# Performance work log

Hardware: AMD Instinct MI355X
Metric: run time of the kernel (lower is better)

## Reference

```python
import jax, jax.numpy as jnp
import numpy as np

ATTEN = 2  # window half-size -> 2*ATTEN+1 = 5 neighbors
B, S, IN, H, MID, OUT = 1024, 100, 100, 128, 32, 2
MAX_LEN = 100
SQRT_H = float(np.sqrt(float(H)))


def _xavier(k, i, o):
    return jax.random.normal(k, (i, o), jnp.float32) * np.sqrt(2.0 / (i + o))


def _positional_encoding():
    pos = np.arange(MAX_LEN, dtype=np.float32)[:, None]
    div = np.exp(np.arange(0, H, 2, dtype=np.float32) * (-np.log(10000.0) / H))
    pe = np.zeros((MAX_LEN, H), np.float32)
    pe[:, 0::2] = np.sin(pos * div)
    pe[:, 1::2] = np.cos(pos * div)
    return jnp.asarray(pe[None])  # (1, MAX_LEN, H)


def setup_inputs() -> dict:
    key = jax.random.key(0)
    ks = jax.random.split(key, 7)
    return {
        "x": jax.random.normal(ks[0], (B, S, IN), jnp.float32),
        "W1": _xavier(ks[1], IN, H),
        "b1": jnp.zeros((1, 1, H), jnp.float32),
        "Wq": _xavier(ks[2], H, H),
        "Wk": _xavier(ks[3], H, H),
        "Wv": _xavier(ks[4], H, H),
        "bv": jnp.zeros((1, 1, H), jnp.float32),
        "W2": _xavier(ks[5], H, MID),
        "b2": jnp.zeros((1, 1, MID), jnp.float32),
        "W3": _xavier(ks[6], MID, OUT),
        "b3": jnp.zeros((1, 1, OUT), jnp.float32),
        "pe": _positional_encoding(),
    }


def reference(x, W1, b1, Wq, Wk, Wv, bv, W2, b2, W3, b3, pe):
    seq_len = x.shape[1]
    h = jax.nn.relu(x @ W1 + b1) + pe[:, :seq_len, :]  # (B,S,H)
    # zero-pad seq dim by ATTEN on each side; torch pad+roll+stack+slice is
    # equivalent to gathering window offsets +2,+1,0,-1,-2 (in that order)
    padded = jnp.pad(h, ((0, 0), (ATTEN, ATTEN), (0, 0)))
    x_nei = jnp.stack(
        [padded[:, ATTEN - k: ATTEN - k + seq_len, :] for k in range(-ATTEN, ATTEN + 1)],
        axis=2,
    )  # (B,S,5,H); index m corresponds to neighbor x[i + ATTEN - m]
    q = h @ Wq                      # (B,S,H)
    keys = x_nei @ Wk               # (B,S,5,H)
    vals = x_nei @ Wv + bv          # (B,S,5,H)
    scores = jnp.einsum("bsh,bswh->bsw", q, keys) / SQRT_H
    w = jax.nn.softmax(scores, axis=-1)  # (B,S,5)
    context = jnp.einsum("bsw,bswh->bsh", w, vals)
    output = jax.nn.relu(context @ W2 + b2) @ W3 + b3  # (B,S,OUT)
    return output, w[:, :, None, :]  # weights shaped (B,S,1,5) like torch
```

## Files before the change

### kernel.cpp

```cpp
#include <hip/hip_runtime.h>
#include <hip/hip_bf16.h>

#define B_ 1024
#define S_ 100
#define IN_ 100
#define H_ 128
#define MID_ 32
#define OUT_ 2
#define P_ (B_ * S_)
#define RSQRT_H 0.08838834764831845f
#define LSTR 136
#define TILE 25
#define KR 32
#define HR 36
#define HTS 40
#define SSTR 36
#define WSTR 40

typedef __attribute__((ext_vector_type(8))) short short8;
typedef __attribute__((ext_vector_type(4))) float float4v;

__device__ __forceinline__ float bf2f(ushort u) {
    union { unsigned u; float f; } c; c.u = ((unsigned)u) << 16; return c.f;
}
__device__ __forceinline__ ushort f2bf(float x) {
    union { float f; unsigned u; } c; c.f = x;
    unsigned r = c.u + 0x7FFFu + ((c.u >> 16) & 1u);
    return (ushort)(r >> 16);
}

__global__ __launch_bounds__(256) void prep_kernel(const float* __restrict__ W1,
                                                   const float* __restrict__ Wv,
                                                   const float* __restrict__ W2,
                                                   const float* __restrict__ Wq,
                                                   const float* __restrict__ Wk,
                                                   ushort* __restrict__ W1T,
                                                   ushort* __restrict__ WvT,
                                                   ushort* __restrict__ W2T,
                                                   ushort* __restrict__ WqkT) {
    int tid = threadIdx.x;
    if (blockIdx.x < 144) {
        int g = blockIdx.x * 256 + tid;
        if (g < 16384) {
            int n = g >> 7, k = g & 127;
            W1T[g] = (k < IN_) ? f2bf(W1[k * H_ + n]) : (ushort)0;
        } else if (g < 32768) {
            int e = g - 16384; int n = e >> 7, k = e & 127;
            WvT[e] = f2bf(Wv[k * H_ + n]);
        } else {
            int e = g - 32768; int n = e >> 7, k = e & 127;
            W2T[e] = f2bf(W2[k * MID_ + n]);
        }
    } else {
        __shared__ float sq[32][132];
        __shared__ float sk[32][132];
        int bb = blockIdx.x - 144;
        int n0 = (bb >> 2) * 32, k0 = (bb & 3) * 32;
        for (int i = tid; i < 32 * 128; i += 256) {
            int r = i >> 7, c = i & 127;
            sq[r][c] = Wq[(k0 + r) * H_ + c];
            sk[r][c] = Wk[(n0 + r) * H_ + c];
        }
        __syncthreads();
        for (int i = tid; i < 1024; i += 256) {
            int kk = i & 31, nn = i >> 5;
            float a = 0.f;
            for (int j = 0; j < 128; ++j) a += sq[kk][j] * sk[nn][j];
            WqkT[(n0 + nn) * 128 + (k0 + kk)] = f2bf(a * RSQRT_H);
        }
    }
}

template <int EPI, bool HT>
__device__ __forceinline__ void mm2(const ushort* __restrict__ A, int abase,
                                    const ushort* __restrict__ WT,
                                    ushort* __restrict__ C,
                                    ushort* __restrict__ hTp,
                                    int wave, int lane,
                                    const float* __restrict__ bias,
                                    const float* __restrict__ pe, int srow0) {
    int l15 = lane & 15, quad = lane >> 4;
    short8 bfrag[2][4];
#pragma unroll
    for (int nt = 0; nt < 2; ++nt) {
        int n = (wave * 2 + nt) * 16 + l15;
#pragma unroll
        for (int ks = 0; ks < 4; ++ks)
            bfrag[nt][ks] = *(const short8*)(WT + n * 128 + ks * 32 + quad * 8);
    }
    float biasv[2] = {0.f, 0.f};
    if (EPI != 0) {
#pragma unroll
        for (int nt = 0; nt < 2; ++nt) biasv[nt] = bias[(wave * 2 + nt) * 16 + l15];
    }
#pragma unroll
    for (int mt = 0; mt < 2; ++mt) {
        short8 afrag[4];
#pragma unroll
        for (int ks = 0; ks < 4; ++ks)
            afrag[ks] = *(const short8*)(A + (abase + mt * 16 + l15) * LSTR + ks * 32 + quad * 8);
#pragma unroll
        for (int nt = 0; nt < 2; ++nt) {
            float4v acc = {0.f, 0.f, 0.f, 0.f};
#pragma unroll
            for (int ks = 0; ks < 4; ++ks)
                acc = __builtin_amdgcn_mfma_f32_16x16x32_bf16(afrag[ks], bfrag[nt][ks], acc, 0, 0, 0);
            int n = (wave * 2 + nt) * 16 + l15;
#pragma unroll
            for (int i = 0; i < 4; ++i) {
                int row = mt * 16 + quad * 4 + i;
                float v = acc[i];
                if (EPI == 1) {
                    int srow = srow0 + row;
                    v = (srow >= 0 && srow < S_)
                            ? (fmaxf(v + biasv[nt], 0.f) + pe[srow * H_ + n]) : 0.f;
                } else if (EPI == 2) v = v + biasv[nt];
                ushort bf = f2bf(v);
                C[row * LSTR + n] = bf;
                if (HT) hTp[n * HTS + row] = bf;
            }
        }
    }
}

__global__ __launch_bounds__(256, 4) void fused_kernel(
    const float* __restrict__ x, const ushort* __restrict__ W1T,
    const ushort* __restrict__ WqkT, const ushort* __restrict__ WvT,
    const ushort* __restrict__ W2T,
    const float* __restrict__ b1, const float* __restrict__ bv,
    const float* __restrict__ b2, const float* __restrict__ W3,
    const float* __restrict__ b3, const float* __restrict__ pe,
    float* __restrict__ out, float* __restrict__ wout) {
    __shared__ __attribute__((aligned(16))) ushort klds[KR * LSTR];
    __shared__ __attribute__((aligned(16))) ushort hlds[HR * LSTR];
    __shared__ __attribute__((aligned(16))) ushort hT[H_ * HTS];
    __shared__ __attribute__((aligned(16))) float  slds[KR * SSTR];
    __shared__ __attribute__((aligned(16))) ushort wband[KR * WSTR];
    __shared__ float warr[TILE * 5];

    int tid = threadIdx.x, wave = tid >> 6, lane = tid & 63;
    int l15 = lane & 15, quad = lane >> 4;
    int b = blockIdx.x >> 2, t = blockIdx.x & 3;
    int r0 = t * TILE;
    int srow0 = r0 - 2;

    for (int i = tid; i < 29 * 18; i += 256) {
        int r = i / 18, c = 100 + 2 * (i - r * 18);
        *(uint*)(klds + r * LSTR + c) = 0u;
    }
    for (int i = tid; i < 3 * 68; i += 256) {
        int r = 29 + i / 68, c = 2 * (i % 68);
        *(uint*)(klds + r * LSTR + c) = 0u;
    }
    for (int i = tid; i < 4 * 68; i += 256) {
        int r = 32 + i / 68, c = 2 * (i % 68);
        *(uint*)(hlds + r * LSTR + c) = 0u;
    }
    {
        int g0 = srow0 < 0 ? 0 : srow0;
        int g1 = (r0 + 27 < S_) ? (r0 + 27) : S_;
        int lr0 = g0 - srow0;
        const float* xb = x + ((size_t)b * S_ + g0) * IN_;
        int pairs = (g1 - g0) * 50;
        for (int p = tid; p < pairs; p += 256) {
            int row = p / 50;
            int c2 = (p - row * 50) * 2;
            const float* src = xb + row * IN_ + c2;
            uint pk = ((uint)f2bf(src[1]) << 16) | (uint)f2bf(src[0]);
            *(uint*)(klds + (lr0 + row) * LSTR + c2) = pk;
        }
    }
    __syncthreads();
    mm2<1, true>(klds, 0, W1T, hlds, hT, wave, lane, b1, pe, srow0);
    __syncthreads();
    mm2<0, false>(hlds, 2, WqkT, klds, nullptr, wave, lane, nullptr, nullptr, 0);
    __syncthreads();
    if (wave < 3) {
        int qt = (wave == 2) ? 1 : 0;
        int ht = (wave == 0) ? 0 : 1;
        short8 afrag[4], bfrag[4];
#pragma unroll
        for (int ks = 0; ks < 4; ++ks) {
            afrag[ks] = *(const short8*)(klds + (qt * 16 + l15) * LSTR + ks * 32 + quad * 8);
            bfrag[ks] = *(const short8*)(hlds + (ht * 16 + l15) * LSTR + ks * 32 + quad * 8);
        }
        float4v acc = {0.f, 0.f, 0.f, 0.f};
#pragma unroll
        for (int ks = 0; ks < 4; ++ks)
            acc = __builtin_amdgcn_mfma_f32_16x16x32_bf16(afrag[ks], bfrag[ks], acc, 0, 0, 0);
#pragma unroll
        for (int i = 0; i < 4; ++i)
            slds[(qt * 16 + quad * 4 + i) * SSTR + ht * 16 + l15] = acc[i];
    } else {
        uint* wz = (uint*)wband;
        for (int i = lane; i < (KR * WSTR) / 2; i += 64) wz[i] = 0u;
    }
    __syncthreads();
    if (tid < TILE) {
        int i = tid;
        float sc5[5];
#pragma unroll
        for (int d = 0; d < 5; ++d) sc5[d] = slds[i * SSTR + i + d];
        float mx = sc5[0];
#pragma unroll
        for (int d = 1; d < 5; ++d) mx = fmaxf(mx, sc5[d]);
        float e5[5], ss = 0.f;
#pragma unroll
        for (int d = 0; d < 5; ++d) { e5[d] = __expf(sc5[d] - mx); ss += e5[d]; }
        float inv = 1.f / ss;
#pragma unroll
        for (int d = 0; d < 5; ++d) {
            float w = e5[d] * inv;
            wband[i * WSTR + i + d] = f2bf(w);
            warr[i * 5 + (4 - d)] = w;
        }
    }
    __syncthreads();
    {
        short8 afr[2];
        afr[0] = *(const short8*)(wband + l15 * WSTR + quad * 8);
        afr[1] = *(const short8*)(wband + (16 + l15) * WSTR + quad * 8);
#pragma unroll
        for (int ntt = 0; ntt < 2; ++ntt) {
            int n = (wave * 2 + ntt) * 16 + l15;
            short8 bfr = *(const short8*)(hT + n * HTS + quad * 8);
#pragma unroll
            for (int mt = 0; mt < 2; ++mt) {
                float4v acc = {0.f, 0.f, 0.f, 0.f};
                acc = __builtin_amdgcn_mfma_f32_16x16x32_bf16(afr[mt], bfr, acc, 0, 0, 0);
#pragma unroll
                for (int i = 0; i < 4; ++i)
                    klds[(mt * 16 + quad * 4 + i) * LSTR + n] = f2bf(acc[i]);
            }
        }
    }
    __syncthreads();
    mm2<2, false>(klds, 0, WvT, hlds, nullptr, wave, lane, bv, nullptr, 0);
    __syncthreads();
    if (tid < TILE * 5)
        wout[(size_t)b * (S_ * 5) + r0 * 5 + tid] = warr[tid];
    {
        int mt = wave & 1, nt = wave >> 1;
        short8 bfrag[4];
#pragma unroll
        for (int ks = 0; ks < 4; ++ks)
            bfrag[ks] = *(const short8*)(W2T + (nt * 16 + l15) * 128 + ks * 32 + quad * 8);
        float bias2 = b2[nt * 16 + l15];
        short8 afrag[4];
#pragma unroll
        for (int ks = 0; ks < 4; ++ks)
            afrag[ks] = *(const short8*)(hlds + (mt * 16 + l15) * LSTR + ks * 32 + quad * 8);
        float4v acc = {0.f, 0.f, 0.f, 0.f};
#pragma unroll
        for (int ks = 0; ks < 4; ++ks)
            acc = __builtin_amdgcn_mfma_f32_16x16x32_bf16(afrag[ks], bfrag[ks], acc, 0, 0, 0);
#pragma unroll
        for (int i = 0; i < 4; ++i) {
            int row = mt * 16 + quad * 4 + i;
            klds[row * LSTR + nt * 16 + l15] = f2bf(fmaxf(acc[i] + bias2, 0.f));
        }
    }
    __syncthreads();
    if (tid < TILE * 2) {
        int r = tid >> 1, c = tid & 1;
        float o = b3[c];
        const ushort* mr = klds + r * LSTR;
#pragma unroll
        for (int cs = 0; cs < 4; ++cs) {
            short8 v = *(const short8*)(mr + cs * 8);
#pragma unroll
            for (int j = 0; j < 8; ++j) o += bf2f((ushort)v[j]) * W3[(cs * 8 + j) * 2 + c];
        }
        out[((size_t)b * S_ + r0 + r) * OUT_ + c] = o;
    }
}

extern "C" void kernel_launch(void* const* d_in, const int* in_sizes, int n_in,
                              void* d_out, int out_size, void* d_ws, size_t ws_size,
                              hipStream_t stream) {
    const float* x  = (const float*)d_in[0];
    const float* W1 = (const float*)d_in[1];
    const float* b1 = (const float*)d_in[2];
    const float* Wq = (const float*)d_in[3];
    const float* Wk = (const float*)d_in[4];
    const float* Wv = (const float*)d_in[5];
    const float* bv = (const float*)d_in[6];
    const float* W2 = (const float*)d_in[7];
    const float* b2 = (const float*)d_in[8];
    const float* W3 = (const float*)d_in[9];
    const float* b3 = (const float*)d_in[10];
    const float* pe = (const float*)d_in[11];

    float* out  = (float*)d_out;
    float* wout = out + (size_t)P_ * OUT_;

    ushort* W1T  = (ushort*)d_ws;
    ushort* WqkT = W1T + 16384;
    ushort* WvT  = WqkT + 16384;
    ushort* W2T  = WvT + 16384;

    prep_kernel<<<160, 256, 0, stream>>>(W1, Wv, W2, Wq, Wk, W1T, WvT, W2T, WqkT);
    fused_kernel<<<B_ * 4, 256, 0, stream>>>(x, W1T, WqkT, WvT, W2T,
                                             b1, bv, b2, W3, b3, pe, out, wout);
}
```

Measured before the change: 168.2 us.

## Fold Wv into W2, fuse softmax and context per wave, vectorize loads

Precomputes Wv·W2 and bv·W2+b2 in the prep kernel, so the per-tile 128x128 value projection is dropped and the context feeds straight into the 32-wide MID layer. Scores, softmax and the banded context matmul now run inside two waves with no block barriers in between. The scores matrix is cut to the needed diagonal band and weights are written straight to global memory. Also vectorizes the x load with float4, packs the hT transposed stores, and shrinks LDS padding strides. Folding the matrices changes bf16 rounding slightly, and the stride changes may alter LDS bank conflicts.

```diff
diff --git a/kernel.cpp b/kernel.cpp
--- a/kernel.cpp
+++ b/kernel.cpp
@@ -9,13 +9,13 @@
 #define OUT_ 2
 #define P_ (B_ * S_)
 #define RSQRT_H 0.08838834764831845f
-#define LSTR 136
+#define LSTR 132
 #define TILE 25
 #define KR 32
-#define HR 36
-#define HTS 40
-#define SSTR 36
-#define WSTR 40
+#define HR 34
+#define HTS 36
+#define WSTR 36
+#define SSC 20
 
 typedef __attribute__((ext_vector_type(8))) short short8;
 typedef __attribute__((ext_vector_type(4))) float float4v;
@@ -30,31 +30,25 @@
 }
 
 __global__ __launch_bounds__(256) void prep_kernel(const float* __restrict__ W1,
+                                                   const float* __restrict__ Wq,
+                                                   const float* __restrict__ Wk,
                                                    const float* __restrict__ Wv,
                                                    const float* __restrict__ W2,
-                                                   const float* __restrict__ Wq,
-                                                   const float* __restrict__ Wk,
+                                                   const float* __restrict__ bv,
+                                                   const float* __restrict__ b2,
                                                    ushort* __restrict__ W1T,
-                                                   ushort* __restrict__ WvT,
-                                                   ushort* __restrict__ W2T,
-                                                   ushort* __restrict__ WqkT) {
+                                                   ushort* __restrict__ WqkT,
+                                                   ushort* __restrict__ Wvw2T,
+                                                   float* __restrict__ bv2) {
     int tid = threadIdx.x;
-    if (blockIdx.x < 144) {
+    if (blockIdx.x < 64) {
         int g = blockIdx.x * 256 + tid;
-        if (g < 16384) {
-            int n = g >> 7, k = g & 127;
-            W1T[g] = (k < IN_) ? f2bf(W1[k * H_ + n]) : (ushort)0;
-        } else if (g < 32768) {
-            int e = g - 16384; int n = e >> 7, k = e & 127;
-            WvT[e] = f2bf(Wv[k * H_ + n]);
-        } else {
-            int e = g - 32768; int n = e >> 7, k = e & 127;
-            W2T[e] = f2bf(W2[k * MID_ + n]);
-        }
-    } else {
+        int n = g >> 7, k = g & 127;
+        W1T[g] = (k < IN_) ? f2bf(W1[k * H_ + n]) : (ushort)0;
+    } else if (blockIdx.x < 80) {
         __shared__ float sq[32][132];
         __shared__ float sk[32][132];
-        int bb = blockIdx.x - 144;
+        int bb = blockIdx.x - 64;
         int n0 = (bb >> 2) * 32, k0 = (bb & 3) * 32;
         for (int i = tid; i < 32 * 128; i += 256) {
             int r = i >> 7, c = i & 127;
@@ -67,6 +61,18 @@
             float a = 0.f;
             for (int j = 0; j < 128; ++j) a += sq[kk][j] * sk[nn][j];
             WqkT[(n0 + nn) * 128 + (k0 + kk)] = f2bf(a * RSQRT_H);
+        }
+    } else if (blockIdx.x < 96) {
+        int e = (blockIdx.x - 80) * 256 + tid;
+        int n = e >> 7, k = e & 127;
+        float a = 0.f;
+        for (int j = 0; j < 128; ++j) a += Wv[k * H_ + j] * W2[j * MID_ + n];
+        Wvw2T[e] = f2bf(a);
+    } else {
+        if (tid < MID_) {
+            float a = b2[tid];
+            for (int j = 0; j < 128; ++j) a += bv[j] * W2[j * MID_ + tid];
+            bv2[tid] = a;
         }
     }
 }
@@ -89,7 +95,7 @@
             bfrag[nt][ks] = *(const short8*)(WT + n * 128 + ks * 32 + quad * 8);
     }
     float biasv[2] = {0.f, 0.f};
-    if (EPI != 0) {
+    if (EPI == 1) {
 #pragma unroll
         for (int nt = 0; nt < 2; ++nt) biasv[nt] = bias[(wave * 2 + nt) * 16 + l15];
     }
@@ -106,6 +112,7 @@
             for (int ks = 0; ks < 4; ++ks)
                 acc = __builtin_amdgcn_mfma_f32_16x16x32_bf16(afrag[ks], bfrag[nt][ks], acc, 0, 0, 0);
             int n = (wave * 2 + nt) * 16 + l15;
+            ushort bfv[4];
 #pragma unroll
             for (int i = 0; i < 4; ++i) {
                 int row = mt * 16 + quad * 4 + i;
@@ -114,10 +121,15 @@
                     int srow = srow0 + row;
                     v = (srow >= 0 && srow < S_)
                             ? (fmaxf(v + biasv[nt], 0.f) + pe[srow * H_ + n]) : 0.f;
-                } else if (EPI == 2) v = v + biasv[nt];
-                ushort bf = f2bf(v);
-                C[row * LSTR + n] = bf;
-                if (HT) hTp[n * HTS + row] = bf;
+                }
+                bfv[i] = f2bf(v);
+                C[row * LSTR + n] = bfv[i];
+            }
+            if (HT) {
+                uint2 pk;
+                pk.x = (uint)bfv[0] | ((uint)bfv[1] << 16);
+                pk.y = (uint)bfv[2] | ((uint)bfv[3] << 16);
+                *(uint2*)(hTp + n * HTS + mt * 16 + quad * 4) = pk;
             }
         }
     }
@@ -125,18 +137,16 @@
 
 __global__ __launch_bounds__(256, 4) void fused_kernel(
     const float* __restrict__ x, const ushort* __restrict__ W1T,
-    const ushort* __restrict__ WqkT, const ushort* __restrict__ WvT,
-    const ushort* __restrict__ W2T,
-    const float* __restrict__ b1, const float* __restrict__ bv,
-    const float* __restrict__ b2, const float* __restrict__ W3,
+    const ushort* __restrict__ WqkT, const ushort* __restrict__ Wvw2T,
+    const float* __restrict__ bv2,
+    const float* __restrict__ b1, const float* __restrict__ W3,
     const float* __restrict__ b3, const float* __restrict__ pe,
     float* __restrict__ out, float* __restrict__ wout) {
     __shared__ __attribute__((aligned(16))) ushort klds[KR * LSTR];
     __shared__ __attribute__((aligned(16))) ushort hlds[HR * LSTR];
     __shared__ __attribute__((aligned(16))) ushort hT[H_ * HTS];
-    __shared__ __attribute__((aligned(16))) float  slds[KR * SSTR];
     __shared__ __attribute__((aligned(16))) ushort wband[KR * WSTR];
-    __shared__ float warr[TILE * 5];
+    __shared__ __attribute__((aligned(16))) float  sscr[2][16][SSC];
 
     int tid = threadIdx.x, wave = tid >> 6, lane = tid & 63;
     int l15 = lane & 15, quad = lane >> 4;
@@ -144,30 +154,43 @@
     int r0 = t * TILE;
     int srow0 = r0 - 2;
 
-    for (int i = tid; i < 29 * 18; i += 256) {
-        int r = i / 18, c = 100 + 2 * (i - r * 18);
+    for (int i = tid; i < 29 * 14; i += 256) {
+        int r = i / 14, c = 100 + 2 * (i - r * 14);
         *(uint*)(klds + r * LSTR + c) = 0u;
     }
-    for (int i = tid; i < 3 * 68; i += 256) {
-        int r = 29 + i / 68, c = 2 * (i % 68);
+    for (int i = tid; i < 3 * 66; i += 256) {
+        int r = 29 + i / 66, c = 2 * (i % 66);
         *(uint*)(klds + r * LSTR + c) = 0u;
     }
-    for (int i = tid; i < 4 * 68; i += 256) {
-        int r = 32 + i / 68, c = 2 * (i % 68);
+    for (int i = tid; i < 2 * 66; i += 256) {
+        int r = 32 + i / 66, c = 2 * (i % 66);
         *(uint*)(hlds + r * LSTR + c) = 0u;
     }
+    for (int i = tid; i < (KR * WSTR) / 2; i += 256)
+        ((uint*)wband)[i] = 0u;
+
     {
         int g0 = srow0 < 0 ? 0 : srow0;
         int g1 = (r0 + 27 < S_) ? (r0 + 27) : S_;
         int lr0 = g0 - srow0;
         const float* xb = x + ((size_t)b * S_ + g0) * IN_;
-        int pairs = (g1 - g0) * 50;
-        for (int p = tid; p < pairs; p += 256) {
-            int row = p / 50;
-            int c2 = (p - row * 50) * 2;
-            const float* src = xb + row * IN_ + c2;
-            uint pk = ((uint)f2bf(src[1]) << 16) | (uint)f2bf(src[0]);
-            *(uint*)(klds + (lr0 + row) * LSTR + c2) = pk;
+        int quads = (g1 - g0) * 25;
+        float4 v[3];
+#pragma unroll
+        for (int it = 0; it < 3; ++it) {
+            int p = tid + it * 256;
+            if (p < quads) v[it] = *(const float4*)(xb + (p / 25) * IN_ + (p % 25) * 4);
+        }
+#pragma unroll
+        for (int it = 0; it < 3; ++it) {
+            int p = tid + it * 256;
+            if (p < quads) {
+                int row = p / 25, qr = p - row * 25;
+                uint2 pk;
+                pk.x = (uint)f2bf(v[it].x) | ((uint)f2bf(v[it].y) << 16);
+                pk.y = (uint)f2bf(v[it].z) | ((uint)f2bf(v[it].w) << 16);
+                *(uint2*)(klds + (lr0 + row) * LSTR + qr * 4) = pk;
+            }
         }
     }
     __syncthreads();
@@ -175,81 +198,73 @@
     __syncthreads();
     mm2<0, false>(hlds, 2, WqkT, klds, nullptr, wave, lane, nullptr, nullptr, 0);
     __syncthreads();
-    if (wave < 3) {
-        int qt = (wave == 2) ? 1 : 0;
-        int ht = (wave == 0) ? 0 : 1;
-        short8 afrag[4], bfrag[4];
-#pragma unroll
-        for (int ks = 0; ks < 4; ++ks) {
+    if (wave < 2) {
+        int qt = wave;
+        short8 afrag[4];
+#pragma unroll
+        for (int ks = 0; ks < 4; ++ks)
             afrag[ks] = *(const short8*)(klds + (qt * 16 + l15) * LSTR + ks * 32 + quad * 8);
-            bfrag[ks] = *(const short8*)(hlds + (ht * 16 + l15) * LSTR + ks * 32 + quad * 8);
-        }
-        float4v acc = {0.f, 0.f, 0.f, 0.f};
-#pragma unroll
-        for (int ks = 0; ks < 4; ++ks)
-            acc = __builtin_amdgcn_mfma_f32_16x16x32_bf16(afrag[ks], bfrag[ks], acc, 0, 0, 0);
-#pragma unroll
-        for (int i = 0; i < 4; ++i)
-            slds[(qt * 16 + quad * 4 + i) * SSTR + ht * 16 + l15] = acc[i];
-    } else {
-        uint* wz = (uint*)wband;
-        for (int i = lane; i < (KR * WSTR) / 2; i += 64) wz[i] = 0u;
-    }
-    __syncthreads();
-    if (tid < TILE) {
-        int i = tid;
-        float sc5[5];
-#pragma unroll
-        for (int d = 0; d < 5; ++d) sc5[d] = slds[i * SSTR + i + d];
-        float mx = sc5[0];
-#pragma unroll
-        for (int d = 1; d < 5; ++d) mx = fmaxf(mx, sc5[d]);
-        float e5[5], ss = 0.f;
-#pragma unroll
-        for (int d = 0; d < 5; ++d) { e5[d] = __expf(sc5[d] - mx); ss += e5[d]; }
-        float inv = 1.f / ss;
-#pragma unroll
-        for (int d = 0; d < 5; ++d) {
-            float w = e5[d] * inv;
-            wband[i * WSTR + i + d] = f2bf(w);
-            warr[i * 5 + (4 - d)] = w;
-        }
-    }
-    __syncthreads();
-    {
-        short8 afr[2];
-        afr[0] = *(const short8*)(wband + l15 * WSTR + quad * 8);
-        afr[1] = *(const short8*)(wband + (16 + l15) * WSTR + quad * 8);
-#pragma unroll
-        for (int ntt = 0; ntt < 2; ++ntt) {
-            int n = (wave * 2 + ntt) * 16 + l15;
-            short8 bfr = *(const short8*)(hT + n * HTS + quad * 8);
-#pragma unroll
-            for (int mt = 0; mt < 2; ++mt) {
-                float4v acc = {0.f, 0.f, 0.f, 0.f};
-                acc = __builtin_amdgcn_mfma_f32_16x16x32_bf16(afr[mt], bfr, acc, 0, 0, 0);
-#pragma unroll
-                for (int i = 0; i < 4; ++i)
-                    klds[(mt * 16 + quad * 4 + i) * LSTR + n] = f2bf(acc[i]);
-            }
-        }
-    }
-    __syncthreads();
-    mm2<2, false>(klds, 0, WvT, hlds, nullptr, wave, lane, bv, nullptr, 0);
-    __syncthreads();
-    if (tid < TILE * 5)
-        wout[(size_t)b * (S_ * 5) + r0 * 5 + tid] = warr[tid];
+#pragma unroll
+        for (int ht = 0; ht < 2; ++ht) {
+            if (ht < qt) continue;
+            short8 bfrag[4];
+#pragma unroll
+            for (int ks = 0; ks < 4; ++ks)
+                bfrag[ks] = *(const short8*)(hlds + (ht * 16 + l15) * LSTR + ks * 32 + quad * 8);
+            float4v acc = {0.f, 0.f, 0.f, 0.f};
+#pragma unroll
+            for (int ks = 0; ks < 4; ++ks)
+                acc = __builtin_amdgcn_mfma_f32_16x16x32_bf16(afrag[ks], bfrag[ks], acc, 0, 0, 0);
+            int c = (ht - qt) * 16 + l15;
+            if (c < SSC) {
+#pragma unroll
+                for (int i = 0; i < 4; ++i) sscr[qt][quad * 4 + i][c] = acc[i];
+            }
+        }
+        int nq = (qt == 0) ? 16 : 9;
+        if (lane < nq) {
+            int q = qt * 16 + lane;
+            float sc5[5];
+#pragma unroll
+            for (int d = 0; d < 5; ++d) sc5[d] = sscr[qt][lane][lane + d];
+            float mx = sc5[0];
+#pragma unroll
+            for (int d = 1; d < 5; ++d) mx = fmaxf(mx, sc5[d]);
+            float e5[5], ss = 0.f;
+#pragma unroll
+            for (int d = 0; d < 5; ++d) { e5[d] = __expf(sc5[d] - mx); ss += e5[d]; }
+            float inv = 1.f / ss;
+            float* wp = wout + ((size_t)b * S_ + r0 + q) * 5;
+#pragma unroll
+            for (int d = 0; d < 5; ++d) {
+                float w = e5[d] * inv;
+                wband[q * WSTR + q + d] = f2bf(w);
+                wp[4 - d] = w;
+            }
+        }
+        short8 wfrag = *(const short8*)(wband + (qt * 16 + l15) * WSTR + quad * 8);
+#pragma unroll
+        for (int nt2 = 0; nt2 < 8; ++nt2) {
+            short8 bfr = *(const short8*)(hT + (nt2 * 16 + l15) * HTS + quad * 8);
+            float4v acc = {0.f, 0.f, 0.f, 0.f};
+            acc = __builtin_amdgcn_mfma_f32_16x16x32_bf16(wfrag, bfr, acc, 0, 0, 0);
+#pragma unroll
+            for (int i = 0; i < 4; ++i)
+                klds[(qt * 16 + quad * 4 + i) * LSTR + nt2 * 16 + l15] = f2bf(acc[i]);
+        }
+    }
+    __syncthreads();
     {
         int mt = wave & 1, nt = wave >> 1;
         short8 bfrag[4];
 #pragma unroll
         for (int ks = 0; ks < 4; ++ks)
-            bfrag[ks] = *(const short8*)(W2T + (nt * 16 + l15) * 128 + ks * 32 + quad * 8);
-        float bias2 = b2[nt * 16 + l15];
+            bfrag[ks] = *(const short8*)(Wvw2T + (nt * 16 + l15) * 128 + ks * 32 + quad * 8);
+        float bias2 = bv2[nt * 16 + l15];
         short8 afrag[4];
 #pragma unroll
         for (int ks = 0; ks < 4; ++ks)
-            afrag[ks] = *(const short8*)(hlds + (mt * 16 + l15) * LSTR + ks * 32 + quad * 8);
+            afrag[ks] = *(const short8*)(klds + (mt * 16 + l15) * LSTR + ks * 32 + quad * 8);
         float4v acc = {0.f, 0.f, 0.f, 0.f};
 #pragma unroll
         for (int ks = 0; ks < 4; ++ks)
@@ -257,21 +272,21 @@
 #pragma unroll
         for (int i = 0; i < 4; ++i) {
             int row = mt * 16 + quad * 4 + i;
-            klds[row * LSTR + nt * 16 + l15] = f2bf(fmaxf(acc[i] + bias2, 0.f));
+            hlds[row * LSTR + nt * 16 + l15] = f2bf(fmaxf(acc[i] + bias2, 0.f));
         }
     }
     __syncthreads();
     if (tid < TILE * 2) {
-        int r = tid >> 1, c = tid & 1;
-        float o = b3[c];
-        const ushort* mr = klds + r * LSTR;
+        int r = tid >> 1, cc = tid & 1;
+        float o = b3[cc];
+        const ushort* mr = hlds + r * LSTR;
 #pragma unroll
         for (int cs = 0; cs < 4; ++cs) {
             short8 v = *(const short8*)(mr + cs * 8);
 #pragma unroll
-            for (int j = 0; j < 8; ++j) o += bf2f((ushort)v[j]) * W3[(cs * 8 + j) * 2 + c];
-        }
-        out[((size_t)b * S_ + r0 + r) * OUT_ + c] = o;
+            for (int j = 0; j < 8; ++j) o += bf2f((ushort)v[j]) * W3[(cs * 8 + j) * 2 + cc];
+        }
+        out[((size_t)b * S_ + r0 + r) * OUT_ + cc] = o;
     }
 }
 
@@ -294,12 +309,13 @@
     float* out  = (float*)d_out;
     float* wout = out + (size_t)P_ * OUT_;
 
-    ushort* W1T  = (ushort*)d_ws;
-    ushort* WqkT = W1T + 16384;
-    ushort* WvT  = WqkT + 16384;
-    ushort* W2T  = WvT + 16384;
-
-    prep_kernel<<<160, 256, 0, stream>>>(W1, Wv, W2, Wq, Wk, W1T, WvT, W2T, WqkT);
-    fused_kernel<<<B_ * 4, 256, 0, stream>>>(x, W1T, WqkT, WvT, W2T,
-                                             b1, bv, b2, W3, b3, pe, out, wout);
-}
+    ushort* W1T   = (ushort*)d_ws;
+    ushort* WqkT  = W1T + 16384;
+    ushort* Wvw2T = WqkT + 16384;
+    float*  bv2   = (float*)(Wvw2T + 4096);
+
+    prep_kernel<<<97, 256, 0, stream>>>(W1, Wq, Wk, Wv, W2, bv, b2,
+                                        W1T, WqkT, Wvw2T, bv2);
+    fused_kernel<<<B_ * 4, 256, 0, stream>>>(x, W1T, WqkT, Wvw2T, bv2,
+                                             b1, W3, b3, pe, out, wout);
+}
```

Measured after the change: 160.6 us. 1.05x faster.
